# Kernel tuning notes

Hardware: AMD Instinct MI355X
Metric: run time of the kernel (lower is better)

Reference implementation:

```python
import jax, jax.numpy as jnp
import numpy as np

EMBED = 1024
HEADS = 16
HEAD_DIM = EMBED // HEADS
B, S = 2, 2048


def setup_inputs() -> dict:
    key = jax.random.key(0)
    k1, k2, k3 = jax.random.split(key, 3)
    scale = 1.0 / np.sqrt(EMBED)
    x = jax.random.normal(k1, (B, S, EMBED), dtype=jnp.float32)
    mask = jnp.ones((B, 1, 1, S), dtype=jnp.int32)
    Wqkv = jax.random.normal(k2, (3 * EMBED, EMBED), dtype=jnp.float32) * scale
    bqkv = jnp.zeros((3 * EMBED,), dtype=jnp.float32)
    Wout = jax.random.normal(k3, (EMBED, EMBED), dtype=jnp.float32) * scale
    bout = jnp.zeros((EMBED,), dtype=jnp.float32)
    return {"x": x, "mask": mask, "Wqkv": Wqkv, "bqkv": bqkv, "Wout": Wout, "bout": bout}


def reference(x, mask, Wqkv, bqkv, Wout, bout):
    Bsz, Sl, E = x.shape
    # fused QKV projection (torch Linear: x @ W.T + b)
    qkv = x @ Wqkv.T + bqkv                      # [B, S, 3E]
    qkv = qkv.reshape(Bsz, Sl, 3, HEADS, HEAD_DIM)
    qkv = jnp.transpose(qkv, (0, 2, 3, 1, 4))    # [B, 3, H, S, D]
    q, k, v = qkv[:, 0], qkv[:, 1], qkv[:, 2]    # each [B, H, S, D]
    scores = jnp.einsum("bhqd,bhkd->bhqk", q, k) / np.sqrt(HEAD_DIM)
    scores = jnp.where(mask == 0, -jnp.inf, scores)  # mask broadcasts [B,1,1,S]
    attn = jax.nn.softmax(scores, axis=-1)       # dropout is identity at eval
    out = jnp.einsum("bhqk,bhkd->bhqd", attn, v) # [B, H, S, D]
    out = jnp.transpose(out, (0, 2, 1, 3)).reshape(Bsz, Sl, E)
    return out @ Wout.T + bout
```

## Files before the change

### kernel.cpp

```cpp
#include <hip/hip_runtime.h>
#include <stdint.h>

typedef unsigned short u16;
typedef __bf16    bf16x8 __attribute__((ext_vector_type(8)));
typedef u16       u16x8  __attribute__((ext_vector_type(8)));
typedef u16       u16x4  __attribute__((ext_vector_type(4)));
typedef float     f32x4  __attribute__((ext_vector_type(4)));
typedef uint32_t  u32x4  __attribute__((ext_vector_type(4)));

#define MFMA16x16x32(a, b, c) __builtin_amdgcn_mfma_f32_16x16x32_bf16((a), (b), (c), 0, 0, 0)

__device__ __forceinline__ u16 f2bf(float f) {
  uint32_t u = __float_as_uint(f);
  u += 0x7FFFu + ((u >> 16) & 1u);
  return (u16)(u >> 16);
}

__device__ __forceinline__ uint32_t pktrunc(float a, float b) {
  return __builtin_amdgcn_perm(__float_as_uint(b), __float_as_uint(a), 0x07060302u);
}

__device__ __forceinline__ bf16x8 ldfrag(const u16* p) {
  return __builtin_bit_cast(bf16x8, *(const u16x8*)p);
}

__device__ __forceinline__ bf16x8 ldfrag2(const u16* p) {
  uint2 a = *(const uint2*)p;
  uint2 b = *(const uint2*)(p + 4);
  u32x4 t; t[0] = a.x; t[1] = a.y; t[2] = b.x; t[3] = b.y;
  return __builtin_bit_cast(bf16x8, t);
}

__device__ __forceinline__ void gl2lds16(const u16* g, u16* l) {
  __builtin_amdgcn_global_load_lds(
      (__attribute__((address_space(1))) void*)g,
      (__attribute__((address_space(3))) void*)l, 16, 0, 0);
}

__global__ __launch_bounds__(256) void convert3(
    const float* __restrict__ x, const float* __restrict__ wq,
    const float* __restrict__ wo, u16* __restrict__ xb,
    u16* __restrict__ wqb, u16* __restrict__ wob) {
  const int NX = (4096 * 1024) / 8;
  const int NQ = (3072 * 1024) / 8;
  int i = blockIdx.x * 256 + threadIdx.x;
  const float* s;
  u16* d;
  if (i < NX)           { s = x;  d = xb;  }
  else if (i < NX + NQ) { s = wq; d = wqb; i -= NX; }
  else                  { s = wo; d = wob; i -= NX + NQ; }
  f32x4 a = ((const f32x4*)s)[2 * (size_t)i];
  f32x4 b = ((const f32x4*)s)[2 * (size_t)i + 1];
  u16x8 r;
  #pragma unroll
  for (int e = 0; e < 4; ++e) { r[e] = f2bf(a[e]); r[4 + e] = f2bf(b[e]); }
  ((u16x8*)d)[i] = r;
}

__global__ __launch_bounds__(256) void qkv_gemm(
    const u16* __restrict__ A, const u16* __restrict__ Bw,
    const float* __restrict__ bias, u16* __restrict__ Qo,
    u16* __restrict__ Ko, u16* __restrict__ Vo) {
  __shared__ __align__(16) u16 As[128 * 64];
  __shared__ __align__(16) u16 Bs[128 * 64];

  const int t = threadIdx.x;
  const int lane = t & 63, w = t >> 6;
  const int quad = lane >> 4, col = lane & 15;
  const int wm = w & 1, wn = w >> 1;
  const int m0 = blockIdx.y * 128, n0 = blockIdx.x * 128;

  f32x4 acc[4][4] = {};

  for (int kt = 0; kt < 16; ++kt) {
    const int ko = kt * 64;
    __syncthreads();
    #pragma unroll
    for (int p = 0; p < 4; ++p) {
      int c = t + 256 * p;
      int r = c >> 3, cc = c & 7;
      int so = ko + ((cc ^ (r & 7)) * 8);
      gl2lds16(A  + (size_t)(m0 + r) * 1024 + so, As + c * 8);
      gl2lds16(Bw + (size_t)(n0 + r) * 1024 + so, Bs + c * 8);
    }
    __syncthreads();

    #pragma unroll
    for (int kk = 0; kk < 2; ++kk) {
      const int e8 = ((kk * 4 + quad) ^ (col & 7)) * 8;
      bf16x8 bfr[4];
      #pragma unroll
      for (int j = 0; j < 4; ++j)
        bfr[j] = ldfrag(Bs + (wn * 64 + j * 16 + col) * 64 + e8);
      #pragma unroll
      for (int i = 0; i < 4; ++i) {
        bf16x8 afr = ldfrag(As + (wm * 64 + i * 16 + col) * 64 + e8);
        #pragma unroll
        for (int j = 0; j < 4; ++j)
          acc[i][j] = MFMA16x16x32(bfr[j], afr, acc[i][j]);
      }
    }
  }

  const int nb = n0 + wn * 64;
  const int which = nb >> 10;
  const int h = (nb >> 6) & 15;
  u16* dst = (which == 0) ? Qo : ((which == 1) ? Ko : Vo);
  const float scale = (which == 0) ? 0.125f : 1.0f;

  #pragma unroll
  for (int j = 0; j < 4; ++j) {
    const f32x4 b4 = *(const f32x4*)(bias + nb + j * 16 + quad * 4);
    #pragma unroll
    for (int i = 0; i < 4; ++i) {
      const int m = m0 + wm * 64 + i * 16 + col;
      const int bb = m >> 11, s = m & 2047;
      u16x4 vv;
      #pragma unroll
      for (int r = 0; r < 4; ++r) vv[r] = f2bf((acc[i][j][r] + b4[r]) * scale);
      *(u16x4*)(dst + ((size_t)(bb * 16 + h) * 2048 + s) * 64 + j * 16 + quad * 4) = vv;
    }
  }
}

__global__ __launch_bounds__(256) void transpose64(
    const u16* __restrict__ V, u16* __restrict__ Vt) {
  __shared__ u16 tile[64][72];
  const int t = threadIdx.x;
  const int s0 = blockIdx.x * 64;
  const int bh = blockIdx.y;
  const u16* Vb = V + (size_t)bh * (2048 * 64);
  u16* Vtb = Vt + (size_t)bh * (64 * 2048);
  #pragma unroll
  for (int p = 0; p < 2; ++p) {
    int c = t + 256 * p;
    int r = c >> 3, c8 = (c & 7) * 8;
    u16x8 v = *(const u16x8*)(Vb + (size_t)(s0 + r) * 64 + c8);
    #pragma unroll
    for (int e = 0; e < 8; ++e) tile[r][c8 + e] = v[e];
  }
  __syncthreads();
  #pragma unroll
  for (int p = 0; p < 2; ++p) {
    int c = t + 256 * p;
    int dr = c >> 3, c8 = (c & 7) * 8;
    u16x8 v;
    #pragma unroll
    for (int e = 0; e < 8; ++e) v[e] = tile[c8 + e][dr];
    *(u16x8*)(Vtb + (size_t)dr * 2048 + s0 + c8) = v;
  }
}

__global__ __launch_bounds__(512, 4) void attn(
    const u16* __restrict__ Q, const u16* __restrict__ K,
    const u16* __restrict__ Vt, const int* __restrict__ mask,
    u16* __restrict__ AO) {
  __shared__ __align__(16) u16 Ks[2][128 * 64];
  __shared__ __align__(16) u16 Ps[8][32 * 68];

  const int t = threadIdx.x;
  const int lane = t & 63, w = t >> 6;
  const int quad = lane >> 4, col = lane & 15;
  const int g = w & 1, u = w >> 1;
  const int bh = blockIdx.x, qb = blockIdx.y;
  const int b = bh >> 4, h = bh & 15;

  const u16* Qh = Q + (size_t)bh * (2048 * 64);
  const u16* Kh = K + (size_t)bh * (2048 * 64);
  const u16* Vh = Vt + (size_t)bh * (64 * 2048);
  const int* mb = mask + b * 2048;

  u16x8 ou;
  #pragma unroll
  for (int e = 0; e < 8; ++e) ou[e] = 0x3F80;
  const bf16x8 ones = __builtin_bit_cast(bf16x8, ou);

  const int qw = qb * 128 + u * 32;
  const int keyg = g * 64;
  const u16* Vl = Vh + (size_t)col * 2048 + keyg + quad * 8;

  bf16x8 aQ[2][2];
  #pragma unroll
  for (int ct = 0; ct < 2; ++ct) {
    #pragma unroll
    for (int kh = 0; kh < 2; ++kh)
      aQ[ct][kh] = ldfrag(Qh + (size_t)(qw + ct * 16 + col) * 64 + kh * 32 + quad * 8);
  }

  f32x4 o[2][4] = {};
  f32x4 lacc[2] = {};
  u16* Pw = &Ps[w][0];

  #pragma unroll
  for (int p = 0; p < 2; ++p) {
    int c = t + 512 * p;
    int kr = c >> 3, kc = c & 7;
    gl2lds16(Kh + (size_t)kr * 64 + ((kc ^ (kr & 7)) * 8), &Ks[0][0] + c * 8);
  }
  __syncthreads();

  for (int kb = 0; kb < 16; ++kb) {
    const int key0 = kb * 128;
    const u16* cur = &Ks[kb & 1][0];

    uint32_t M[4][2];
    #pragma unroll
    for (int jj = 0; jj < 4; ++jj) {
      int4 m4 = *(const int4*)(mb + key0 + keyg + jj * 16 + quad * 4);
      M[jj][0] = (m4.x ? 0x0000FFFFu : 0u) | (m4.y ? 0xFFFF0000u : 0u);
      M[jj][1] = (m4.z ? 0x0000FFFFu : 0u) | (m4.w ? 0xFFFF0000u : 0u);
    }
    __builtin_amdgcn_sched_barrier(0);

    if (kb < 15) {
      u16* nxt = &Ks[(kb + 1) & 1][0];
      #pragma unroll
      for (int p = 0; p < 2; ++p) {
        int c = t + 512 * p;
        int kr = c >> 3, kc = c & 7;
        gl2lds16(Kh + (size_t)(key0 + 128 + kr) * 64 + ((kc ^ (kr & 7)) * 8), nxt + c * 8);
      }
    }

    f32x4 sc[2][4] = {};
    #pragma unroll
    for (int j = 0; j < 4; ++j) {
      #pragma unroll
      for (int kh = 0; kh < 2; ++kh) {
        bf16x8 ak = ldfrag(cur + (keyg + j * 16 + col) * 64 + (((kh * 4 + quad) ^ (col & 7)) * 8));
        sc[0][j] = MFMA16x16x32(ak, aQ[0][kh], sc[0][j]);
        sc[1][j] = MFMA16x16x32(ak, aQ[1][kh], sc[1][j]);
      }
    }

    #pragma unroll
    for (int jj = 0; jj < 4; ++jj) {
      #pragma unroll
      for (int ct = 0; ct < 2; ++ct) {
        uint2 pk;
        pk.x = pktrunc(__expf(sc[ct][jj][0]), __expf(sc[ct][jj][1])) & M[jj][0];
        pk.y = pktrunc(__expf(sc[ct][jj][2]), __expf(sc[ct][jj][3])) & M[jj][1];
        *(uint2*)(Pw + (ct * 16 + col) * 68 + jj * 16 + quad * 4) = pk;
      }
    }

    #pragma unroll
    for (int jp = 0; jp < 2; ++jp) {
      bf16x8 bP0 = ldfrag2(Pw + col * 68 + jp * 32 + quad * 8);
      bf16x8 bP1 = ldfrag2(Pw + (16 + col) * 68 + jp * 32 + quad * 8);
      lacc[0] = MFMA16x16x32(ones, bP0, lacc[0]);
      lacc[1] = MFMA16x16x32(ones, bP1, lacc[1]);
      #pragma unroll
      for (int dt = 0; dt < 4; ++dt) {
        bf16x8 av = ldfrag(Vl + dt * 32768 + key0 + jp * 32);
        o[0][dt] = MFMA16x16x32(av, bP0, o[0][dt]);
        o[1][dt] = MFMA16x16x32(av, bP1, o[1][dt]);
      }
    }

    __syncthreads();
  }

  float* Rb = (float*)(&Ps[0][0]);
  float* Ro = Rb + u * 2048 + lane * 32;
  float* Rl = Rb + 8192 + u * 128 + lane * 2;
  if (g == 1) {
    #pragma unroll
    for (int ct = 0; ct < 2; ++ct)
      #pragma unroll
      for (int dt = 0; dt < 4; ++dt)
        *(f32x4*)(Ro + ((ct * 4 + dt) ^ (lane & 7)) * 4) = o[ct][dt];
    Rl[0] = lacc[0][0]; Rl[1] = lacc[1][0];
  }
  __syncthreads();
  if (g == 0) {
    float rl[2];
    #pragma unroll
    for (int ct = 0; ct < 2; ++ct) {
      #pragma unroll
      for (int dt = 0; dt < 4; ++dt)
        o[ct][dt] += *(const f32x4*)(Ro + ((ct * 4 + dt) ^ (lane & 7)) * 4);
      rl[ct] = 1.0f / (lacc[ct][0] + Rl[ct]);
    }
    #pragma unroll
    for (int ct = 0; ct < 2; ++ct) {
      const int q = qw + ct * 16 + col;
      #pragma unroll
      for (int dt = 0; dt < 4; ++dt) {
        u16x4 v;
        #pragma unroll
        for (int r = 0; r < 4; ++r) v[r] = f2bf(o[ct][dt][r] * rl[ct]);
        *(u16x4*)(AO + (size_t)(b * 2048 + q) * 1024 + h * 64 + dt * 16 + quad * 4) = v;
      }
    }
  }
}

__global__ __launch_bounds__(256) void proj_gemm(
    const u16* __restrict__ A, const u16* __restrict__ Bw,
    const float* __restrict__ bias, float* __restrict__ out) {
  __shared__ __align__(16) u16 As[2][128 * 64];
  __shared__ __align__(16) u16 Bs[2][64 * 64];

  const int t = threadIdx.x;
  const int lane = t & 63, w = t >> 6;
  const int quad = lane >> 4, col = lane & 15;
  const int wm = w & 1, wn = w >> 1;
  const int m0 = blockIdx.y * 128, n0 = blockIdx.x * 64;

  f32x4 acc[4][2] = {};

  #pragma unroll
  for (int p = 0; p < 4; ++p) {
    int c = t + 256 * p;
    int r = c >> 3, cc = c & 7;
    gl2lds16(A + (size_t)(m0 + r) * 1024 + ((cc ^ (r & 7)) * 8), &As[0][0] + c * 8);
  }
  #pragma unroll
  for (int p = 0; p < 2; ++p) {
    int c = t + 256 * p;
    int r = c >> 3, cc = c & 7;
    gl2lds16(Bw + (size_t)(n0 + r) * 1024 + ((cc ^ (r & 7)) * 8), &Bs[0][0] + c * 8);
  }
  __syncthreads();

  for (int kt = 0; kt < 16; ++kt) {
    const u16* Ac = &As[kt & 1][0];
    const u16* Bc = &Bs[kt & 1][0];
    if (kt < 15) {
      const int ko = (kt + 1) * 64;
      u16* An = &As[(kt + 1) & 1][0];
      u16* Bn = &Bs[(kt + 1) & 1][0];
      #pragma unroll
      for (int p = 0; p < 4; ++p) {
        int c = t + 256 * p;
        int r = c >> 3, cc = c & 7;
        gl2lds16(A + (size_t)(m0 + r) * 1024 + ko + ((cc ^ (r & 7)) * 8), An + c * 8);
      }
      #pragma unroll
      for (int p = 0; p < 2; ++p) {
        int c = t + 256 * p;
        int r = c >> 3, cc = c & 7;
        gl2lds16(Bw + (size_t)(n0 + r) * 1024 + ko + ((cc ^ (r & 7)) * 8), Bn + c * 8);
      }
    }

    #pragma unroll
    for (int kk = 0; kk < 2; ++kk) {
      const int e8 = ((kk * 4 + quad) ^ (col & 7)) * 8;
      bf16x8 bfr[2];
      #pragma unroll
      for (int j = 0; j < 2; ++j)
        bfr[j] = ldfrag(Bc + (wn * 32 + j * 16 + col) * 64 + e8);
      #pragma unroll
      for (int i = 0; i < 4; ++i) {
        bf16x8 afr = ldfrag(Ac + (wm * 64 + i * 16 + col) * 64 + e8);
        #pragma unroll
        for (int j = 0; j < 2; ++j)
          acc[i][j] = MFMA16x16x32(bfr[j], afr, acc[i][j]);
      }
    }
    __syncthreads();
  }

  const int nb = n0 + wn * 32;
  #pragma unroll
  for (int j = 0; j < 2; ++j) {
    const f32x4 b4 = *(const f32x4*)(bias + nb + j * 16 + quad * 4);
    #pragma unroll
    for (int i = 0; i < 4; ++i) {
      const int m = m0 + wm * 64 + i * 16 + col;
      f32x4 vv = acc[i][j] + b4;
      *(f32x4*)(out + (size_t)m * 1024 + nb + j * 16 + quad * 4) = vv;
    }
  }
}

extern "C" void kernel_launch(void* const* d_in, const int* in_sizes, int n_in,
                              void* d_out, int out_size, void* d_ws, size_t ws_size,
                              hipStream_t stream) {
  (void)in_sizes; (void)n_in; (void)out_size; (void)ws_size;
  const float* x    = (const float*)d_in[0];
  const int*   mask = (const int*)d_in[1];
  const float* Wqkv = (const float*)d_in[2];
  const float* bqkv = (const float*)d_in[3];
  const float* Wout = (const float*)d_in[4];
  const float* bout = (const float*)d_in[5];
  float* out = (float*)d_out;
  char* ws = (char*)d_ws;

  u16* Xb  = (u16*)(ws);
  u16* Wqb = (u16*)(ws + ((size_t)8  << 20));
  u16* Wob = (u16*)(ws + ((size_t)14 << 20));
  u16* Qb  = (u16*)(ws + ((size_t)16 << 20));
  u16* Kb  = (u16*)(ws + ((size_t)24 << 20));
  u16* Vb  = (u16*)(ws + ((size_t)32 << 20));
  u16* Vtb = (u16*)(ws + ((size_t)40 << 20));
  u16* AO  = Xb;

  convert3<<<dim3(4096), dim3(256), 0, stream>>>(x, Wqkv, Wout, Xb, Wqb, Wob);
  qkv_gemm<<<dim3(24, 32), dim3(256), 0, stream>>>(Xb, Wqb, bqkv, Qb, Kb, Vb);
  transpose64<<<dim3(32, 32), dim3(256), 0, stream>>>(Vb, Vtb);
  attn<<<dim3(32, 16), dim3(512), 0, stream>>>(Qb, Kb, Vtb, mask, AO);
  proj_gemm<<<dim3(16, 32), dim3(256), 0, stream>>>(AO, Wob, bout, out);
}
```

Before: 223.4 us.

## Double-buffer QKV GEMM tiles and stage V through LDS in attention

The QKV GEMM now uses two LDS buffers, prefetching the next K-slice while computing on the current one, which removes one barrier per iteration. The attention kernel stages V tiles into double-buffered, XOR-swizzled LDS with async loads instead of reading V fragments straight from global memory. The P scratch buffer is shrunk and swizzled and is now processed in two 32-key halves, and the mask conversion is deferred until after the QK MFMAs. This raises LDS use (about 64KB in attention), which may cut occupancy below the 4-block launch bound.

Result: faster. 207.0 us (-7.4%).

```diff
diff --git a/kernel.cpp b/kernel.cpp
--- a/kernel.cpp
+++ b/kernel.cpp
@@ -24,9 +24,9 @@
   return __builtin_bit_cast(bf16x8, *(const u16x8*)p);
 }
 
-__device__ __forceinline__ bf16x8 ldfrag2(const u16* p) {
-  uint2 a = *(const uint2*)p;
-  uint2 b = *(const uint2*)(p + 4);
+__device__ __forceinline__ bf16x8 ldfrag2b(const u16* p0, const u16* p1) {
+  uint2 a = *(const uint2*)p0;
+  uint2 b = *(const uint2*)p1;
   u32x4 t; t[0] = a.x; t[1] = a.y; t[2] = b.x; t[3] = b.y;
   return __builtin_bit_cast(bf16x8, t);
 }
@@ -61,8 +61,8 @@
     const u16* __restrict__ A, const u16* __restrict__ Bw,
     const float* __restrict__ bias, u16* __restrict__ Qo,
     u16* __restrict__ Ko, u16* __restrict__ Vo) {
-  __shared__ __align__(16) u16 As[128 * 64];
-  __shared__ __align__(16) u16 Bs[128 * 64];
+  __shared__ __align__(16) u16 As[2][128 * 64];
+  __shared__ __align__(16) u16 Bs[2][128 * 64];
 
   const int t = threadIdx.x;
   const int lane = t & 63, w = t >> 6;
@@ -72,18 +72,32 @@
 
   f32x4 acc[4][4] = {};
 
+  #pragma unroll
+  for (int p = 0; p < 4; ++p) {
+    int c = t + 256 * p;
+    int r = c >> 3, cc = c & 7;
+    int so = (cc ^ (r & 7)) * 8;
+    gl2lds16(A  + (size_t)(m0 + r) * 1024 + so, &As[0][0] + c * 8);
+    gl2lds16(Bw + (size_t)(n0 + r) * 1024 + so, &Bs[0][0] + c * 8);
+  }
+  __syncthreads();
+
   for (int kt = 0; kt < 16; ++kt) {
-    const int ko = kt * 64;
-    __syncthreads();
-    #pragma unroll
-    for (int p = 0; p < 4; ++p) {
-      int c = t + 256 * p;
-      int r = c >> 3, cc = c & 7;
-      int so = ko + ((cc ^ (r & 7)) * 8);
-      gl2lds16(A  + (size_t)(m0 + r) * 1024 + so, As + c * 8);
-      gl2lds16(Bw + (size_t)(n0 + r) * 1024 + so, Bs + c * 8);
-    }
-    __syncthreads();
+    const u16* Ac = &As[kt & 1][0];
+    const u16* Bc = &Bs[kt & 1][0];
+    if (kt < 15) {
+      const int ko = (kt + 1) * 64;
+      u16* An = &As[(kt + 1) & 1][0];
+      u16* Bn = &Bs[(kt + 1) & 1][0];
+      #pragma unroll
+      for (int p = 0; p < 4; ++p) {
+        int c = t + 256 * p;
+        int r = c >> 3, cc = c & 7;
+        int so = ko + ((cc ^ (r & 7)) * 8);
+        gl2lds16(A  + (size_t)(m0 + r) * 1024 + so, An + c * 8);
+        gl2lds16(Bw + (size_t)(n0 + r) * 1024 + so, Bn + c * 8);
+      }
+    }
 
     #pragma unroll
     for (int kk = 0; kk < 2; ++kk) {
@@ -91,15 +105,16 @@
       bf16x8 bfr[4];
       #pragma unroll
       for (int j = 0; j < 4; ++j)
-        bfr[j] = ldfrag(Bs + (wn * 64 + j * 16 + col) * 64 + e8);
+        bfr[j] = ldfrag(Bc + (wn * 64 + j * 16 + col) * 64 + e8);
       #pragma unroll
       for (int i = 0; i < 4; ++i) {
-        bf16x8 afr = ldfrag(As + (wm * 64 + i * 16 + col) * 64 + e8);
+        bf16x8 afr = ldfrag(Ac + (wm * 64 + i * 16 + col) * 64 + e8);
         #pragma unroll
         for (int j = 0; j < 4; ++j)
           acc[i][j] = MFMA16x16x32(bfr[j], afr, acc[i][j]);
       }
     }
+    __syncthreads();
   }
 
   const int nb = n0 + wn * 64;
@@ -156,7 +171,8 @@
     const u16* __restrict__ Vt, const int* __restrict__ mask,
     u16* __restrict__ AO) {
   __shared__ __align__(16) u16 Ks[2][128 * 64];
-  __shared__ __align__(16) u16 Ps[8][32 * 68];
+  __shared__ __align__(16) u16 Vs[2][64 * 128];
+  __shared__ __align__(16) u16 Ps[8][32 * 32];
 
   const int t = threadIdx.x;
   const int lane = t & 63, w = t >> 6;
@@ -177,7 +193,6 @@
 
   const int qw = qb * 128 + u * 32;
   const int keyg = g * 64;
-  const u16* Vl = Vh + (size_t)col * 2048 + keyg + quad * 8;
 
   bf16x8 aQ[2][2];
   #pragma unroll
@@ -196,29 +211,32 @@
     int c = t + 512 * p;
     int kr = c >> 3, kc = c & 7;
     gl2lds16(Kh + (size_t)kr * 64 + ((kc ^ (kr & 7)) * 8), &Ks[0][0] + c * 8);
+    int vr = c >> 4, vc = c & 15;
+    gl2lds16(Vh + (size_t)vr * 2048 + ((vc ^ (vr & 15)) * 8), &Vs[0][0] + c * 8);
   }
   __syncthreads();
 
   for (int kb = 0; kb < 16; ++kb) {
     const int key0 = kb * 128;
-    const u16* cur = &Ks[kb & 1][0];
-
-    uint32_t M[4][2];
-    #pragma unroll
-    for (int jj = 0; jj < 4; ++jj) {
-      int4 m4 = *(const int4*)(mb + key0 + keyg + jj * 16 + quad * 4);
-      M[jj][0] = (m4.x ? 0x0000FFFFu : 0u) | (m4.y ? 0xFFFF0000u : 0u);
-      M[jj][1] = (m4.z ? 0x0000FFFFu : 0u) | (m4.w ? 0xFFFF0000u : 0u);
-    }
+    const u16* Kc = &Ks[kb & 1][0];
+    const u16* Vc = &Vs[kb & 1][0];
+
+    int4 m4[4];
+    #pragma unroll
+    for (int jj = 0; jj < 4; ++jj)
+      m4[jj] = *(const int4*)(mb + key0 + keyg + jj * 16 + quad * 4);
     __builtin_amdgcn_sched_barrier(0);
 
     if (kb < 15) {
-      u16* nxt = &Ks[(kb + 1) & 1][0];
+      u16* Kn = &Ks[(kb + 1) & 1][0];
+      u16* Vn = &Vs[(kb + 1) & 1][0];
       #pragma unroll
       for (int p = 0; p < 2; ++p) {
         int c = t + 512 * p;
         int kr = c >> 3, kc = c & 7;
-        gl2lds16(Kh + (size_t)(key0 + 128 + kr) * 64 + ((kc ^ (kr & 7)) * 8), nxt + c * 8);
+        gl2lds16(Kh + (size_t)(key0 + 128 + kr) * 64 + ((kc ^ (kr & 7)) * 8), Kn + c * 8);
+        int vr = c >> 4, vc = c & 15;
+        gl2lds16(Vh + (size_t)vr * 2048 + key0 + 128 + ((vc ^ (vr & 15)) * 8), Vn + c * 8);
       }
     }
 
@@ -227,32 +245,45 @@
     for (int j = 0; j < 4; ++j) {
       #pragma unroll
       for (int kh = 0; kh < 2; ++kh) {
-        bf16x8 ak = ldfrag(cur + (keyg + j * 16 + col) * 64 + (((kh * 4 + quad) ^ (col & 7)) * 8));
+        bf16x8 ak = ldfrag(Kc + (keyg + j * 16 + col) * 64 + (((kh * 4 + quad) ^ (col & 7)) * 8));
         sc[0][j] = MFMA16x16x32(ak, aQ[0][kh], sc[0][j]);
         sc[1][j] = MFMA16x16x32(ak, aQ[1][kh], sc[1][j]);
       }
     }
 
+    uint32_t M[4][2];
     #pragma unroll
     for (int jj = 0; jj < 4; ++jj) {
-      #pragma unroll
-      for (int ct = 0; ct < 2; ++ct) {
-        uint2 pk;
-        pk.x = pktrunc(__expf(sc[ct][jj][0]), __expf(sc[ct][jj][1])) & M[jj][0];
-        pk.y = pktrunc(__expf(sc[ct][jj][2]), __expf(sc[ct][jj][3])) & M[jj][1];
-        *(uint2*)(Pw + (ct * 16 + col) * 68 + jj * 16 + quad * 4) = pk;
-      }
-    }
-
-    #pragma unroll
-    for (int jp = 0; jp < 2; ++jp) {
-      bf16x8 bP0 = ldfrag2(Pw + col * 68 + jp * 32 + quad * 8);
-      bf16x8 bP1 = ldfrag2(Pw + (16 + col) * 68 + jp * 32 + quad * 8);
+      M[jj][0] = (m4[jj].x ? 0x0000FFFFu : 0u) | (m4[jj].y ? 0xFFFF0000u : 0u);
+      M[jj][1] = (m4[jj].z ? 0x0000FFFFu : 0u) | (m4[jj].w ? 0xFFFF0000u : 0u);
+    }
+
+    #pragma unroll
+    for (int sp = 0; sp < 2; ++sp) {
+      #pragma unroll
+      for (int jj = 0; jj < 2; ++jj) {
+        const int j = sp * 2 + jj;
+        #pragma unroll
+        for (int ct = 0; ct < 2; ++ct) {
+          uint2 pk;
+          pk.x = pktrunc(__expf(sc[ct][j][0]), __expf(sc[ct][j][1])) & M[j][0];
+          pk.y = pktrunc(__expf(sc[ct][j][2]), __expf(sc[ct][j][3])) & M[j][1];
+          const int q = ct * 16 + col;
+          const int s = (jj * 4 + quad) ^ (q & 7);
+          *(uint2*)(Pw + q * 32 + s * 4) = pk;
+        }
+      }
+
+      bf16x8 bP0 = ldfrag2b(Pw + col * 32 + (((quad * 2) ^ (col & 7)) * 4),
+                            Pw + col * 32 + (((quad * 2 + 1) ^ (col & 7)) * 4));
+      bf16x8 bP1 = ldfrag2b(Pw + (16 + col) * 32 + (((quad * 2) ^ (col & 7)) * 4),
+                            Pw + (16 + col) * 32 + (((quad * 2 + 1) ^ (col & 7)) * 4));
       lacc[0] = MFMA16x16x32(ones, bP0, lacc[0]);
       lacc[1] = MFMA16x16x32(ones, bP1, lacc[1]);
+      const int win = g * 2 + sp;
       #pragma unroll
       for (int dt = 0; dt < 4; ++dt) {
-        bf16x8 av = ldfrag(Vl + dt * 32768 + key0 + jp * 32);
+        bf16x8 av = ldfrag(Vc + (dt * 16 + col) * 128 + (((win * 4 + quad) ^ col) * 8));
         o[0][dt] = MFMA16x16x32(av, bP0, o[0][dt]);
         o[1][dt] = MFMA16x16x32(av, bP1, o[1][dt]);
       }
@@ -261,9 +292,8 @@
     __syncthreads();
   }
 
-  float* Rb = (float*)(&Ps[0][0]);
-  float* Ro = Rb + u * 2048 + lane * 32;
-  float* Rl = Rb + 8192 + u * 128 + lane * 2;
+  float* Ro = (float*)(&Ks[0][0]) + u * 2048 + lane * 32;
+  float* Rl = (float*)(&Vs[0][0]) + u * 128 + lane * 2;
   if (g == 1) {
     #pragma unroll
     for (int ct = 0; ct < 2; ++ct)
```
